# Kernel tuning notes

Measured on AMD Instinct MI355X. Metric: run time of the kernel, lower is better.

The kernel has to match this reference:

```python
import jax, jax.numpy as jnp
import numpy as np

N, C, H, W = 32, 256, 56, 56
G = 16
EPS = 1e-05
N_ITER = 10


def isqrt_newton_schulz(A, num_iters):
    # A: (G, G) SPD. Returns A^{-1/2} via Newton-Schulz iteration.
    dim = A.shape[0]
    normA = jnp.linalg.norm(A)  # Frobenius norm
    Y = A / normA
    I = jnp.eye(dim, dtype=A.dtype)
    Z = jnp.eye(dim, dtype=A.dtype)
    for _ in range(num_iters):
        T = 0.5 * (3.0 * I - Z @ Y)
        Y = Y @ T
        Z = T @ Z
    return Z / jnp.sqrt(normA)


def setup_inputs() -> dict:
    key = jax.random.key(0)
    k1, = jax.random.split(key, 1)
    x = jax.random.normal(k1, (N, C, H, W), dtype=jnp.float32)
    weight = jnp.ones((1, C, 1, 1), dtype=jnp.float32)
    bias = jnp.zeros((1, C, 1, 1), dtype=jnp.float32)
    return {"x": x, "weight": weight, "bias": bias}


def reference(x, weight, bias):
    n, c_all, h, w = x.shape
    c = (c_all // G) * G  # == c_all here (256 divisible by 16)
    # (N, c/G, G, H, W) -> (G, N, c/G, H, W) -> (G, M)
    x1 = x[:, :c].reshape(n, c // G, G, h, w).transpose(2, 0, 1, 3, 4).reshape(G, -1)
    mean1 = jnp.mean(x1, axis=-1, keepdims=True)  # (G, 1)
    xc = x1 - mean1
    M = xc.shape[1]
    cov = xc @ xc.T / M + EPS * jnp.eye(G, dtype=x.dtype)  # (G, G)
    decorr = isqrt_newton_schulz(cov, N_ITER)  # (G, G)
    y = decorr @ xc  # (G, M) whitening GEMM
    y = y.reshape(G, n, c // G, h, w).transpose(1, 2, 0, 3, 4).reshape(n, c, h, w)
    return y * weight + bias
```

## Files before the change

### kernel.cpp

```cpp
#include <hip/hip_runtime.h>


constexpr int kC    = 256;
constexpr int kHW   = 3136;
constexpr int kP    = 512;
constexpr int kAcc  = 152;
constexpr float kEps = 1e-5f;
constexpr int kNsIter = 10;
constexpr int kSplit = 4;
constexpr int kChunk = 196;
constexpr int kNB   = kP * 4;
constexpr int kTileF2 = 196;
constexpr int kTileF4 = 98;

typedef float floatx4 __attribute__((ext_vector_type(4)));

__device__ __host__ constexpr int triidx(int j, int k) {
  return j * 16 - (j * (j - 1)) / 2 + (k - j);
}

template <int Ctrl, int RowMask>
__device__ __forceinline__ float dpp_fadd(float x) {
  int perm = __builtin_amdgcn_update_dpp(0, __float_as_int(x), Ctrl, RowMask, 0xf, true);
  return x + __int_as_float(perm);
}
__device__ __forceinline__ float wave_sum64(float x) {
  x = dpp_fadd<0xB1, 0xF>(x);
  x = dpp_fadd<0x4E, 0xF>(x);
  x = dpp_fadd<0x124, 0xF>(x);
  x = dpp_fadd<0x128, 0xF>(x);
  x = dpp_fadd<0x142, 0xA>(x);
  x = dpp_fadd<0x143, 0xC>(x);
  return x;
}

template <int R0, int R1, int R2, int R3>
struct RowSet {
  static constexpr int O0 = 0;
  static constexpr int O1 = O0 + (16 - R0);
  static constexpr int O2 = O1 + (16 - R1);
  static constexpr int O3 = O2 + (16 - R2);
};

template <int R0, int R1, int R2, int R3, int S0>
__device__ __forceinline__ void accum_tile(const float2* __restrict__ lds2, int lane,
                                           float* __restrict__ acc) {
  using RS = RowSet<R0, R1, R2, R3>;
  for (int p = lane; p < kTileF2; p += 64) {
    float2 v[16];
#pragma unroll
    for (int c = 0; c < 16; ++c) v[c] = lds2[c * kTileF2 + p];
#pragma unroll
    for (int c = 0; c < 4; ++c) acc[34 + c] += v[S0 + c].x + v[S0 + c].y;
#pragma unroll
    for (int k = R0; k < 16; ++k) acc[RS::O0 + k - R0] += v[R0].x * v[k].x + v[R0].y * v[k].y;
#pragma unroll
    for (int k = R1; k < 16; ++k) acc[RS::O1 + k - R1] += v[R1].x * v[k].x + v[R1].y * v[k].y;
#pragma unroll
    for (int k = R2; k < 16; ++k) acc[RS::O2 + k - R2] += v[R2].x * v[k].x + v[R2].y * v[k].y;
#pragma unroll
    for (int k = R3; k < 16; ++k) acc[RS::O3 + k - R3] += v[R3].x * v[k].x + v[R3].y * v[k].y;
  }
}

template <int R0, int R1, int R2, int R3, int S0>
__device__ __forceinline__ void write_acc(float* __restrict__ pT, int blk, int lane,
                                          const float* __restrict__ acc) {
  using RS = RowSet<R0, R1, R2, R3>;
#pragma unroll
  for (int k = R0; k < 16; ++k) {
    float r = wave_sum64(acc[RS::O0 + k - R0]);
    if (lane == 63) pT[(size_t)(16 + triidx(R0, k)) * kNB + blk] = r;
  }
#pragma unroll
  for (int k = R1; k < 16; ++k) {
    float r = wave_sum64(acc[RS::O1 + k - R1]);
    if (lane == 63) pT[(size_t)(16 + triidx(R1, k)) * kNB + blk] = r;
  }
#pragma unroll
  for (int k = R2; k < 16; ++k) {
    float r = wave_sum64(acc[RS::O2 + k - R2]);
    if (lane == 63) pT[(size_t)(16 + triidx(R2, k)) * kNB + blk] = r;
  }
#pragma unroll
  for (int k = R3; k < 16; ++k) {
    float r = wave_sum64(acc[RS::O3 + k - R3]);
    if (lane == 63) pT[(size_t)(16 + triidx(R3, k)) * kNB + blk] = r;
  }
#pragma unroll
  for (int c = 0; c < 4; ++c) {
    float r = wave_sum64(acc[34 + c]);
    if (lane == 63) pT[(size_t)(S0 + c) * kNB + blk] = r;
  }
}

__global__ __launch_bounds__(256, 4) void fd_stats(const float* __restrict__ x,
                                                   float* __restrict__ pT) {
  __shared__ __align__(16) float2 tile[16 * kTileF2];
  const int blk = blockIdx.x;
  const int p = blk >> 2, s = blk & 3;
  const int n = p >> 4, c1 = p & 15;
  const int t = threadIdx.x;
  const int w = __builtin_amdgcn_readfirstlane(t >> 6);
  const int lane = t & 63;

  const float4* xb =
      reinterpret_cast<const float4*>(x) + (size_t)(n * kC + c1 * 16) * (kHW / 4);

  float acc[38];
#pragma unroll
  for (int a = 0; a < 38; ++a) acc[a] = 0.f;

  float4* lds4 = reinterpret_cast<float4*>(tile);
  const float2* lds2 = tile;

  for (int t2 = 0; t2 < 2; ++t2) {
    if (t2) __syncthreads();
    const int fbase = s * 196 + t2 * kTileF4;
    for (int q = t; q < 16 * kTileF4; q += 256) {
      const int ch = q / kTileF4, fo = q - ch * kTileF4;
      lds4[ch * kTileF4 + fo] = xb[(size_t)ch * (kHW / 4) + fbase + fo];
    }
    __syncthreads();
    switch (w) {
      case 0:  accum_tile<0, 1, 14, 15, 0 >(lds2, lane, acc); break;
      case 1:  accum_tile<2, 3, 12, 13, 4 >(lds2, lane, acc); break;
      case 2:  accum_tile<4, 5, 10, 11, 8 >(lds2, lane, acc); break;
      default: accum_tile<6, 7, 8,  9,  12>(lds2, lane, acc); break;
    }
  }
  switch (w) {
    case 0:  write_acc<0, 1, 14, 15, 0 >(pT, blk, lane, acc); break;
    case 1:  write_acc<2, 3, 12, 13, 4 >(pT, blk, lane, acc); break;
    case 2:  write_acc<4, 5, 10, 11, 8 >(pT, blk, lane, acc); break;
    default: write_acc<6, 7, 8,  9,  12>(pT, blk, lane, acc); break;
  }
}

__global__ __launch_bounds__(256) void fd_newton(const float* __restrict__ pT,
                                                 float* __restrict__ params) {
  __shared__ float stats[kAcc];
  __shared__ float meanv[16];
  __shared__ float Yb[2][256];
  __shared__ float Zb[2][256];
  __shared__ float Tm[256];
  __shared__ float redb[4];
  __shared__ float snorm;
  const int t = threadIdx.x;
  const int w = t >> 6, lane = t & 63;

  for (int a = w; a < kAcc; a += 4) {
    const float4* row = reinterpret_cast<const float4*>(pT + (size_t)a * kNB);
    float sum = 0.f;
#pragma unroll
    for (int i = 0; i < kNB / 4 / 64; ++i) {
      float4 v = row[i * 64 + lane];
      sum += (v.x + v.y) + (v.z + v.w);
    }
    float r = wave_sum64(sum);
    if (lane == 63) stats[a] = r;
  }
  __syncthreads();

  constexpr float invM = 1.0f / (float)(kP * kHW);
  if (t < 16) meanv[t] = stats[t] * invM;
  __syncthreads();

  const int i = t >> 4, j = t & 15;
  const int a = i < j ? i : j, b = i < j ? j : i;
  float cij = stats[16 + triidx(a, b)] * invM - meanv[i] * meanv[j];
  if (i == j) cij += kEps;

  float r = wave_sum64(cij * cij);
  if ((t & 63) == 63) redb[t >> 6] = r;
  __syncthreads();
  if (t == 0) snorm = sqrtf((redb[0] + redb[1]) + (redb[2] + redb[3]));
  __syncthreads();

  Yb[0][t] = cij * (1.0f / snorm);
  Zb[0][t] = (i == j) ? 1.0f : 0.0f;
  __syncthreads();

  int cur = 0;
  for (int it = 0; it < kNsIter; ++it) {
    float acc = 0.f;
#pragma unroll
    for (int k = 0; k < 16; ++k) acc += Zb[cur][i * 16 + k] * Yb[cur][k * 16 + j];
    Tm[t] = ((i == j) ? 1.5f : 0.0f) - 0.5f * acc;
    __syncthreads();
    float y = 0.f, z = 0.f;
#pragma unroll
    for (int k = 0; k < 16; ++k) {
      y += Yb[cur][i * 16 + k] * Tm[k * 16 + j];
      z += Tm[i * 16 + k] * Zb[cur][k * 16 + j];
    }
    Yb[cur ^ 1][t] = y;
    Zb[cur ^ 1][t] = z;
    cur ^= 1;
    __syncthreads();
  }

  const float D = Zb[cur][t] / sqrtf(snorm);
  params[t] = D;
  Tm[t] = D * meanv[j];
  __syncthreads();
  if (t < 16) {
    float o = 0.f;
#pragma unroll
    for (int k = 0; k < 16; ++k) o += Tm[t * 16 + k];
    params[256 + t] = o;
  }
}

__global__ __launch_bounds__(256, 4) void fd_whiten(const float* __restrict__ x,
                                                    const float* __restrict__ weight,
                                                    const float* __restrict__ bias,
                                                    const float* __restrict__ params,
                                                    float* __restrict__ out) {
  const int blk = blockIdx.x;
  const int p = blk >> 2, s = blk & (kSplit - 1);
  const int n = p >> 4, c1 = p & 15;
  const int t = threadIdx.x;
  const int w    = __builtin_amdgcn_readfirstlane(t >> 6);
  const int lane = t & 63;
  const int g0   = 4 * w;

  const float* base  = x   + (size_t)(n * kC + c1 * 16) * kHW;
  float*       obase = out + (size_t)(n * kC + c1 * 16) * kHW;

  float d[4][16];
#pragma unroll
  for (int gg = 0; gg < 4; ++gg)
#pragma unroll
    for (int j = 0; j < 16; ++j)
      d[gg][j] = params[(g0 + gg) * 16 + j];

  float wv[4], sv[4];
#pragma unroll
  for (int gg = 0; gg < 4; ++gg) {
    const int g  = g0 + gg;
    const int ch = c1 * 16 + g;
    wv[gg] = weight[ch];
    sv[gg] = bias[ch] - params[256 + g] * wv[gg];
  }

  for (int lp = lane; lp < kChunk; lp += 64) {
    const int pos = s * kChunk + lp;
    float4 acc0 = make_float4(0.f, 0.f, 0.f, 0.f);
    float4 acc1 = acc0, acc2 = acc0, acc3 = acc0;
#pragma unroll
    for (int j = 0; j < 16; ++j) {
      const float4 v = reinterpret_cast<const float4*>(base + j * kHW)[pos];
#define ACC(A, dd) A.x += (dd) * v.x; A.y += (dd) * v.y; A.z += (dd) * v.z; A.w += (dd) * v.w;
      ACC(acc0, d[0][j]); ACC(acc1, d[1][j]); ACC(acc2, d[2][j]); ACC(acc3, d[3][j]);
#undef ACC
    }
#define EMIT(A, gg)                                                          \
    {                                                                        \
      floatx4 o;                                                             \
      o.x = A.x * wv[gg] + sv[gg]; o.y = A.y * wv[gg] + sv[gg];              \
      o.z = A.z * wv[gg] + sv[gg]; o.w = A.w * wv[gg] + sv[gg];              \
      __builtin_nontemporal_store(                                           \
          o, reinterpret_cast<floatx4*>(obase + (g0 + gg) * kHW) + pos);     \
    }
    EMIT(acc0, 0) EMIT(acc1, 1) EMIT(acc2, 2) EMIT(acc3, 3)
#undef EMIT
  }
}

extern "C" void kernel_launch(void* const* d_in, const int* in_sizes, int n_in,
                              void* d_out, int out_size, void* d_ws, size_t ws_size,
                              hipStream_t stream) {
  const float* x      = (const float*)d_in[0];
  const float* weight = (const float*)d_in[1];
  const float* bias   = (const float*)d_in[2];
  float* out = (float*)d_out;

  float* wsf      = (float*)d_ws;
  float* partials = wsf;
  float* params   = wsf + (size_t)kAcc * kNB;

  fd_stats <<<kNB, 256, 0, stream>>>(x, partials);
  fd_newton<<<1,   256, 0, stream>>>(partials, params);
  fd_whiten<<<kP * kSplit, 256, 0, stream>>>(x, weight, bias, params, out);
}
```

Baseline: 105.1 us.

## Prefetch second stats tile into registers and parallelize partial-sum reduction

The stats kernel now stages the second tile's global loads in registers while the first tile is being accumulated from LDS, so global load latency overlaps with compute. The reduction of 2048 per-block partials per statistic moves out of the single-block Newton kernel into a new 152-block reduce kernel. The Newton kernel then just reads the 152 reduced stats. This adds a kernel launch and more register pressure in the stats kernel, in exchange for less serialized work in the one-block kernel.

```diff
diff --git a/kernel.cpp b/kernel.cpp
--- a/kernel.cpp
+++ b/kernel.cpp
@@ -12,6 +12,7 @@
 constexpr int kNB   = kP * 4;
 constexpr int kTileF2 = 196;
 constexpr int kTileF4 = 98;
+constexpr int kStage  = 7;
 
 typedef float floatx4 __attribute__((ext_vector_type(4)));
 
@@ -114,21 +115,49 @@
   float4* lds4 = reinterpret_cast<float4*>(tile);
   const float2* lds2 = tile;
 
-  for (int t2 = 0; t2 < 2; ++t2) {
-    if (t2) __syncthreads();
-    const int fbase = s * 196 + t2 * kTileF4;
-    for (int q = t; q < 16 * kTileF4; q += 256) {
-      const int ch = q / kTileF4, fo = q - ch * kTileF4;
-      lds4[ch * kTileF4 + fo] = xb[(size_t)ch * (kHW / 4) + fbase + fo];
-    }
-    __syncthreads();
-    switch (w) {
-      case 0:  accum_tile<0, 1, 14, 15, 0 >(lds2, lane, acc); break;
-      case 1:  accum_tile<2, 3, 12, 13, 4 >(lds2, lane, acc); break;
-      case 2:  accum_tile<4, 5, 10, 11, 8 >(lds2, lane, acc); break;
-      default: accum_tile<6, 7, 8,  9,  12>(lds2, lane, acc); break;
-    }
-  }
+  float4 stg[kStage];
+#define LOAD_REGS(t2)                                                     \
+  {                                                                       \
+    const int fbase = s * 196 + (t2) * kTileF4;                           \
+    _Pragma("unroll")                                                     \
+    for (int i = 0; i < kStage; ++i) {                                    \
+      const int q = t + i * 256;                                          \
+      if (q < 16 * kTileF4) {                                             \
+        const int ch = q / kTileF4, fo = q - ch * kTileF4;                \
+        stg[i] = xb[(size_t)ch * (kHW / 4) + fbase + fo];                 \
+      }                                                                   \
+    }                                                                     \
+  }
+#define WRITE_LDS()                                                       \
+  {                                                                       \
+    _Pragma("unroll")                                                     \
+    for (int i = 0; i < kStage; ++i) {                                    \
+      const int q = t + i * 256;                                          \
+      if (q < 16 * kTileF4) lds4[q] = stg[i];                             \
+    }                                                                     \
+  }
+#define COMPUTE()                                                         \
+  switch (w) {                                                            \
+    case 0:  accum_tile<0, 1, 14, 15, 0 >(lds2, lane, acc); break;        \
+    case 1:  accum_tile<2, 3, 12, 13, 4 >(lds2, lane, acc); break;        \
+    case 2:  accum_tile<4, 5, 10, 11, 8 >(lds2, lane, acc); break;        \
+    default: accum_tile<6, 7, 8,  9,  12>(lds2, lane, acc); break;        \
+  }
+
+  LOAD_REGS(0)
+  WRITE_LDS()
+  __syncthreads();
+  LOAD_REGS(1)
+  COMPUTE()
+  __syncthreads();
+  WRITE_LDS()
+  __syncthreads();
+  COMPUTE()
+
+#undef LOAD_REGS
+#undef WRITE_LDS
+#undef COMPUTE
+
   switch (w) {
     case 0:  write_acc<0, 1, 14, 15, 0 >(pT, blk, lane, acc); break;
     case 1:  write_acc<2, 3, 12, 13, 4 >(pT, blk, lane, acc); break;
@@ -137,7 +166,21 @@
   }
 }
 
-__global__ __launch_bounds__(256) void fd_newton(const float* __restrict__ pT,
+__global__ __launch_bounds__(256) void fd_reduce(const float* __restrict__ pT,
+                                                 float* __restrict__ statsg) {
+  __shared__ float wbuf[4];
+  const int a = blockIdx.x;
+  const int t = threadIdx.x, lane = t & 63, w = t >> 6;
+  const float4* row = reinterpret_cast<const float4*>(pT + (size_t)a * kNB);
+  float4 v0 = row[t], v1 = row[t + 256];
+  float sum = ((v0.x + v0.y) + (v0.z + v0.w)) + ((v1.x + v1.y) + (v1.z + v1.w));
+  float r = wave_sum64(sum);
+  if (lane == 63) wbuf[w] = r;
+  __syncthreads();
+  if (t == 0) statsg[a] = (wbuf[0] + wbuf[1]) + (wbuf[2] + wbuf[3]);
+}
+
+__global__ __launch_bounds__(256) void fd_newton(const float* __restrict__ statsg,
                                                  float* __restrict__ params) {
   __shared__ float stats[kAcc];
   __shared__ float meanv[16];
@@ -147,19 +190,8 @@
   __shared__ float redb[4];
   __shared__ float snorm;
   const int t = threadIdx.x;
-  const int w = t >> 6, lane = t & 63;
-
-  for (int a = w; a < kAcc; a += 4) {
-    const float4* row = reinterpret_cast<const float4*>(pT + (size_t)a * kNB);
-    float sum = 0.f;
-#pragma unroll
-    for (int i = 0; i < kNB / 4 / 64; ++i) {
-      float4 v = row[i * 64 + lane];
-      sum += (v.x + v.y) + (v.z + v.w);
-    }
-    float r = wave_sum64(sum);
-    if (lane == 63) stats[a] = r;
-  }
+
+  if (t < kAcc) stats[t] = statsg[t];
   __syncthreads();
 
   constexpr float invM = 1.0f / (float)(kP * kHW);
@@ -278,9 +310,11 @@
 
   float* wsf      = (float*)d_ws;
   float* partials = wsf;
-  float* params   = wsf + (size_t)kAcc * kNB;
-
-  fd_stats <<<kNB, 256, 0, stream>>>(x, partials);
-  fd_newton<<<1,   256, 0, stream>>>(partials, params);
+  float* statsg   = wsf + (size_t)kAcc * kNB;
+  float* params   = statsg + kAcc;
+
+  fd_stats <<<kNB,  256, 0, stream>>>(x, partials);
+  fd_reduce<<<kAcc, 256, 0, stream>>>(partials, statsg);
+  fd_newton<<<1,    256, 0, stream>>>(statsg, params);
   fd_whiten<<<kP * kSplit, 256, 0, stream>>>(x, weight, bias, params, out);
 }
```

Result: slower. 116.6 us (+11.0%).
